# Optimization experiments

Measured on AMD Instinct MI355X. Metric: run time of the kernel, lower is better.

Reference implementation:

```python
import jax, jax.numpy as jnp
import numpy as np

N_NODES = 50000
N_EDGES = 500000
IN_DIM = 64
OUT_DIM = 64
NUM_RELS = 16


def setup_inputs() -> dict:
    key = jax.random.key(0)
    ks = jax.random.split(key, 8)
    h = jax.random.normal(ks[0], (N_NODES, IN_DIM), dtype=jnp.float32)
    he = jax.random.normal(ks[1], (N_EDGES, IN_DIM), dtype=jnp.float32)
    src = jax.random.randint(ks[2], (N_EDGES,), 0, N_NODES)
    dst = jax.random.randint(ks[3], (N_EDGES,), 0, N_NODES)
    rel = jax.random.randint(ks[4], (N_EDGES,), 0, NUM_RELS)
    # xavier-ish scales
    W_shared = jax.random.normal(ks[5], (OUT_DIM, IN_DIM), dtype=jnp.float32) * (2.0 / (IN_DIM + OUT_DIM)) ** 0.5
    W_attn = jax.random.normal(ks[6], (1, 3 * OUT_DIM), dtype=jnp.float32) * (2.0 / (3 * OUT_DIM + 1)) ** 0.5
    W_rel = jax.random.normal(ks[7], (NUM_RELS, IN_DIM, OUT_DIM), dtype=jnp.float32) * (2.0 / (IN_DIM + OUT_DIM)) ** 0.5
    return {"h": h, "he": he, "src": src, "dst": dst, "rel": rel,
            "W_shared": W_shared, "W_attn": W_attn, "W_rel": W_rel}


def reference(h, he, src, dst, rel, W_shared, W_attn, W_rel):
    # --- edge attention: a = attn_fc([z_src, z_edge, z_dst]) (raw linear score, no softmax in original) ---
    Z = h @ W_shared.T                      # [N, out] project all nodes once
    ze = he @ W_shared.T                    # [E, out]
    # split attn weight to avoid materializing [E, 3*out] concat
    Wa_s, Wa_e, Wa_d = jnp.split(W_attn, 3, axis=1)   # each [1, out]
    a = Z[src] @ Wa_s.T + ze @ Wa_e.T + Z[dst] @ Wa_d.T   # [E, 1]
    # --- message: msg = (h_src @ W_rel[rel]) * a ---
    # compute per-(node, relation) transform once [N, R, out], then gather per edge
    H_all = jnp.einsum('ni,rio->nro', h, W_rel)          # [N, R, out]
    msg = H_all[src, rel] * a                             # [E, out]
    # --- scatter-sum aggregation into destination nodes ---
    out = jax.ops.segment_sum(msg, dst, num_segments=N_NODES)  # [N, out]
    # apply_func: activation (relu), no bias
    return jax.nn.relu(out)
```

## Files before the change

kernel.cpp:

```cpp
#include <hip/hip_runtime.h>
#include <math.h>

#define N_NODES 50000
#define N_EDGES 500000
#define NUM_RELS 16
#define GH 64
#define SCAN_BLKS 196
#define AE_BLKS 1954

typedef _Float16 f16x8 __attribute__((ext_vector_type(8)));
typedef _Float16 f16x4 __attribute__((ext_vector_type(4)));
typedef float    f32x4 __attribute__((ext_vector_type(4)));


__global__ void kz(int* __restrict__ c1, int* __restrict__ cu1,
                   int* __restrict__ c2, int* __restrict__ cu2) {
    int i = blockIdx.x * 256 + threadIdx.x;
    if (i < NUM_RELS) { c1[i] = 0; cu1[i] = 0; }
    if (i < N_NODES)  { c2[i] = 0; cu2[i] = 0; }
}

__global__ __launch_bounds__(256) void k_node(
    const float* __restrict__ h, const float4* __restrict__ he4,
    const float* __restrict__ W_shared, const float* __restrict__ W_attn,
    const int* __restrict__ dst, const int* __restrict__ rel,
    float* __restrict__ sn, float* __restrict__ dn,
    int* __restrict__ c1, int* __restrict__ c2,
    _Float16* __restrict__ h_hi, _Float16* __restrict__ h_lo,
    float* __restrict__ edot) {
    __shared__ float sus[64], sud[64], sve[64];
    __shared__ float sdot[256];
    __shared__ int hist[NUM_RELS];
    const int t = threadIdx.x, bid = blockIdx.x;
    const int lane = t & 63;
    const int w = t >> 6;

    const size_t fb = ((size_t)bid * 256 + (size_t)w * 64) * 16;
    const size_t fmax = (size_t)N_EDGES * 16 - 1;
    float4 v[16];
#pragma unroll
    for (int k = 0; k < 16; ++k) {
        size_t fi = fb + (size_t)k * 64 + lane;
        if (fi > fmax) fi = fmax;
        v[k] = he4[fi];
    }

    if (t < 64) {
        float us = 0.f, ud = 0.f, ve = 0.f;
        for (int o = 0; o < 64; ++o) {
            float ww = W_shared[o * 64 + t];
            us = fmaf(ww, W_attn[o],       us);
            ve = fmaf(ww, W_attn[64 + o],  ve);
            ud = fmaf(ww, W_attn[128 + o], ud);
        }
        sus[t] = us; sud[t] = ud; sve[t] = ve;
    }
    if (t < NUM_RELS) hist[t] = 0;
    __syncthreads();

    int n = bid * 256 + t;
    if (bid < SCAN_BLKS && n < N_NODES) {
        const float* hp = h + (size_t)n * 64;
        float s = 0.f, d = 0.f;
#pragma unroll
        for (int i = 0; i < 64; i += 4) {
            float4 hv = *(const float4*)(hp + i);
            s = fmaf(hv.x, sus[i], s);     s = fmaf(hv.y, sus[i + 1], s);
            s = fmaf(hv.z, sus[i + 2], s); s = fmaf(hv.w, sus[i + 3], s);
            d = fmaf(hv.x, sud[i], d);     d = fmaf(hv.y, sud[i + 1], d);
            d = fmaf(hv.z, sud[i + 2], d); d = fmaf(hv.w, sud[i + 3], d);
            f16x4 hi, lo;
            hi[0] = (_Float16)hv.x; lo[0] = (_Float16)(hv.x - (float)hi[0]);
            hi[1] = (_Float16)hv.y; lo[1] = (_Float16)(hv.y - (float)hi[1]);
            hi[2] = (_Float16)hv.z; lo[2] = (_Float16)(hv.z - (float)hi[2]);
            hi[3] = (_Float16)hv.w; lo[3] = (_Float16)(hv.w - (float)hi[3]);
            *(f16x4*)(h_hi + (size_t)n * 64 + i) = hi;
            *(f16x4*)(h_lo + (size_t)n * 64 + i) = lo;
        }
        sn[n] = s; dn[n] = d;
    }

    {
        float4 u = *(const float4*)(sve + 4 * (lane & 15));
#pragma unroll
        for (int k = 0; k < 16; ++k) {
            float p = v[k].x * u.x + v[k].y * u.y + v[k].z * u.z + v[k].w * u.w;
            p += __shfl_xor(p, 1, 64);
            p += __shfl_xor(p, 2, 64);
            p += __shfl_xor(p, 4, 64);
            p += __shfl_xor(p, 8, 64);
            if ((lane & 15) == 0) sdot[w * 64 + k * 4 + (lane >> 4)] = p;
        }
    }
    int e = bid * 256 + t;
    if (e < N_EDGES) edot[e] = sdot[t];

    if (bid < SCAN_BLKS) {
        for (int ee = bid * 256 + t; ee < N_EDGES; ee += SCAN_BLKS * 256) {
            atomicAdd(&hist[rel[ee]], 1);
            atomicAdd(&c2[dst[ee]], 1);
        }
    }
    __syncthreads();
    if (bid < SCAN_BLKS && t < NUM_RELS && hist[t]) atomicAdd(&c1[t], hist[t]);
}

__global__ __launch_bounds__(256) void k_scan1(const int* __restrict__ c2,
                                               int* __restrict__ partial) {
    const int t = threadIdx.x, bid = blockIdx.x;
    const int lane = t & 63, wv = t >> 6;
    __shared__ int ws[4];
    int idx = bid * 256 + t;
    int s = (idx < N_NODES) ? c2[idx] : 0;
#pragma unroll
    for (int off = 32; off > 0; off >>= 1) s += __shfl_xor(s, off, 64);
    if (lane == 0) ws[wv] = s;
    __syncthreads();
    if (t == 0) partial[bid] = ws[0] + ws[1] + ws[2] + ws[3];
}

__global__ __launch_bounds__(256) void k_scan2(const int* __restrict__ partial,
                                               int* __restrict__ pbase,
                                               int* __restrict__ offs2,
                                               const int* __restrict__ c1,
                                               int* __restrict__ offs1) {
    const int t = threadIdx.x;
    const int lane = t & 63, wv = t >> 6;
    __shared__ int wsum[4];
    int v = (t < SCAN_BLKS) ? partial[t] : 0;
    int x = v;
#pragma unroll
    for (int off = 1; off < 64; off <<= 1) {
        int y = __shfl_up(x, off, 64);
        if (lane >= off) x += y;
    }
    if (lane == 63) wsum[wv] = x;
    __syncthreads();
    int wbase = 0;
#pragma unroll
    for (int j = 0; j < 4; ++j) if (j < wv) wbase += wsum[j];
    int excl = wbase + x - v;
    pbase[t] = excl;
    if (t == 255) offs2[N_NODES] = excl;
    if (t == 0) {
        int b = 0;
        for (int r = 0; r < NUM_RELS; ++r) { offs1[r] = b; b += c1[r]; }
        offs1[NUM_RELS] = b;
    }
}

__global__ __launch_bounds__(256) void k_scan3(int* __restrict__ c2,
                                               const int* __restrict__ pbase,
                                               int* __restrict__ offs2) {
    const int t = threadIdx.x, bid = blockIdx.x;
    const int lane = t & 63, wv = t >> 6;
    __shared__ int wsum[4];
    int idx = bid * 256 + t;
    int v = (idx < N_NODES) ? c2[idx] : 0;
    int x = v;
#pragma unroll
    for (int off = 1; off < 64; off <<= 1) {
        int y = __shfl_up(x, off, 64);
        if (lane >= off) x += y;
    }
    if (lane == 63) wsum[wv] = x;
    __syncthreads();
    int wbase = 0;
#pragma unroll
    for (int j = 0; j < 4; ++j) if (j < wv) wbase += wsum[j];
    if (idx < N_NODES) offs2[idx] = pbase[bid] + wbase + x - v;
    if (idx < 4096) c2[idx] = 0;
}

__global__ __launch_bounds__(256) void k_ae(
    const int* __restrict__ src, const int* __restrict__ dst,
    const int* __restrict__ rel, const float* __restrict__ edot,
    const float* __restrict__ sn, const float* __restrict__ dn,
    const int* __restrict__ offs1, int* __restrict__ cur1p,
    const int* __restrict__ offs2, int* __restrict__ cursor2,
    int* __restrict__ srcs, float* __restrict__ aes, int* __restrict__ iperm) {
    __shared__ int hist[NUM_RELS], bbase[NUM_RELS], soffs[NUM_RELS];
    const int t = threadIdx.x;
    const int e = blockIdx.x * 256 + t;
    if (t < NUM_RELS) { hist[t] = 0; soffs[t] = offs1[t]; }
    const bool valid = (e < N_EDGES);
    int r = 0, s_ = 0, d_ = 0;
    float aev = 0.f;
    if (valid) {
        s_ = src[e]; d_ = dst[e]; r = rel[e];
        aev = edot[e] + sn[s_] + dn[d_];
    }
    __syncthreads();
    int lpos = 0;
    if (valid) lpos = atomicAdd(&hist[r], 1);
    __syncthreads();
    if (t < NUM_RELS) bbase[t] = hist[t] ? atomicAdd(&cur1p[t << 8], hist[t]) : 0;
    __syncthreads();
    if (valid) {
        int p1 = soffs[r] + bbase[r] + lpos;
        srcs[p1] = s_; aes[p1] = aev;
        int p2 = offs2[d_] + atomicAdd(&cursor2[d_], 1);
        iperm[p2] = p1;
    }
}

__global__ __launch_bounds__(256, 4) void k_msg(
    const _Float16* __restrict__ h_hi, const _Float16* __restrict__ h_lo,
    const float* __restrict__ W_rel, const int* __restrict__ offs1,
    const int* __restrict__ srcs, const float* __restrict__ aes,
    float* __restrict__ msg)
{
    const int t = threadIdx.x;
    const int lane = t & 63;
    const int quad = lane >> 4;
    const int col  = lane & 15;
    const int wib  = t >> 6;
    const int rh   = blockIdx.x & 31;
    const int r    = rh & 15;
    const int half = rh >> 4;
    const int g    = blockIdx.x >> 5;
    const int wr   = g * 4 + wib;

    const int begin = __builtin_amdgcn_readfirstlane(offs1[r]);
    const int end   = __builtin_amdgcn_readfirstlane(offs1[r + 1]);

    const float* Wb = W_rel + (size_t)r * 4096;
    f16x8 bh[2][2], bl[2][2];
#pragma unroll
    for (int kb = 0; kb < 2; ++kb)
#pragma unroll
        for (int n2 = 0; n2 < 2; ++n2)
#pragma unroll
            for (int j = 0; j < 8; ++j) {
                float w = Wb[(kb * 32 + quad * 8 + j) * 64 + (half * 2 + n2) * 16 + col];
                _Float16 hi = (_Float16)w;
                bh[kb][n2][j] = hi;
                bl[kb][n2][j] = (_Float16)(w - (float)hi);
            }

    for (int base = begin + wr * 16; base < end; base += 256 * 16) {
        int m16 = end - base; if (m16 > 16) m16 = 16;
        const int ridx = base + (col < m16 ? col : m16 - 1);
        const int   sv = srcs[ridx];
        const float av = (col < m16) ? aes[ridx] : 0.f;

        const _Float16* ph = h_hi + (size_t)sv * 64 + quad * 8;
        const _Float16* pl = h_lo + (size_t)sv * 64 + quad * 8;
        f16x8 ah0 = *(const f16x8*)ph, ah1 = *(const f16x8*)(ph + 32);
        f16x8 al0 = *(const f16x8*)pl, al1 = *(const f16x8*)(pl + 32);

        f32x4 acc0 = {0.f, 0.f, 0.f, 0.f};
        f32x4 acc1 = {0.f, 0.f, 0.f, 0.f};
        acc0 = __builtin_amdgcn_mfma_f32_16x16x32_f16(ah0, bh[0][0], acc0, 0, 0, 0);
        acc1 = __builtin_amdgcn_mfma_f32_16x16x32_f16(ah0, bh[0][1], acc1, 0, 0, 0);
        acc0 = __builtin_amdgcn_mfma_f32_16x16x32_f16(ah0, bl[0][0], acc0, 0, 0, 0);
        acc1 = __builtin_amdgcn_mfma_f32_16x16x32_f16(ah0, bl[0][1], acc1, 0, 0, 0);
        acc0 = __builtin_amdgcn_mfma_f32_16x16x32_f16(al0, bh[0][0], acc0, 0, 0, 0);
        acc1 = __builtin_amdgcn_mfma_f32_16x16x32_f16(al0, bh[0][1], acc1, 0, 0, 0);
        acc0 = __builtin_amdgcn_mfma_f32_16x16x32_f16(ah1, bh[1][0], acc0, 0, 0, 0);
        acc1 = __builtin_amdgcn_mfma_f32_16x16x32_f16(ah1, bh[1][1], acc1, 0, 0, 0);
        acc0 = __builtin_amdgcn_mfma_f32_16x16x32_f16(ah1, bl[1][0], acc0, 0, 0, 0);
        acc1 = __builtin_amdgcn_mfma_f32_16x16x32_f16(ah1, bl[1][1], acc1, 0, 0, 0);
        acc0 = __builtin_amdgcn_mfma_f32_16x16x32_f16(al1, bh[1][0], acc0, 0, 0, 0);
        acc1 = __builtin_amdgcn_mfma_f32_16x16x32_f16(al1, bh[1][1], acc1, 0, 0, 0);

#pragma unroll
        for (int reg = 0; reg < 4; ++reg) {
            const int m = quad * 4 + reg;
            const float am = __shfl(av, m, 64);
            if (m < m16) {
                float* op = msg + (size_t)(base + m) * 64 + half * 32 + col;
                op[0]  = am * acc0[reg];
                op[16] = am * acc1[reg];
            }
        }
    }
}

__global__ __launch_bounds__(256) void k_out(
    const float* __restrict__ msg, const int* __restrict__ iperm,
    const int* __restrict__ offs2, float* __restrict__ out)
{
    const int lane = threadIdx.x & 63;
    const int gw   = blockIdx.x * 4 + (threadIdx.x >> 6);
    const int nw   = gridDim.x * 4;
    for (int n = gw; n < N_NODES; n += nw) {
        const int qb = offs2[n], qe = offs2[n + 1];
        float s0 = 0.f, s1 = 0.f, s2 = 0.f, s3 = 0.f;
        int q = qb;
        for (; q + 4 <= qe; q += 4) {
            int p0 = iperm[q], p1 = iperm[q + 1], p2 = iperm[q + 2], p3 = iperm[q + 3];
            s0 += msg[(size_t)p0 * 64 + lane];
            s1 += msg[(size_t)p1 * 64 + lane];
            s2 += msg[(size_t)p2 * 64 + lane];
            s3 += msg[(size_t)p3 * 64 + lane];
        }
        for (; q < qe; ++q)
            s0 += msg[(size_t)iperm[q] * 64 + lane];
        float s = (s0 + s1) + (s2 + s3);
        out[(size_t)n * 64 + lane] = fmaxf(s, 0.f);
    }
}

extern "C" void kernel_launch(void* const* d_in, const int* in_sizes, int n_in,
                              void* d_out, int out_size, void* d_ws, size_t ws_size,
                              hipStream_t stream) {
    const float*  h        = (const float*)d_in[0];
    const float4* he4      = (const float4*)d_in[1];
    const int*    src      = (const int*)d_in[2];
    const int*    dst      = (const int*)d_in[3];
    const int*    rel      = (const int*)d_in[4];
    const float*  W_shared = (const float*)d_in[5];
    const float*  W_attn   = (const float*)d_in[6];
    const float*  W_rel    = (const float*)d_in[7];
    float*        out      = (float*)d_out;

    int*      counts1 = (int*)d_ws + 0;
    int*      cursor1 = (int*)d_ws + 16;
    int*      offs1   = (int*)d_ws + 32;
    int*      counts2 = (int*)d_ws + 64;
    int*      cursor2 = (int*)d_ws + 50064;
    int*      offs2   = (int*)d_ws + 100064;
    float*    sn      = (float*)d_ws + 150080;
    float*    dn      = (float*)d_ws + 200080;
    int*      srcs    = (int*)d_ws + 250080;
    float*    aes     = (float*)d_ws + 750080;
    int*      iperm   = (int*)d_ws + 1250080;
    _Float16* h_hi    = (_Float16*)((int*)d_ws + 1750080);
    _Float16* h_lo    = (_Float16*)((int*)d_ws + 3350080);
    float*    edot    = (float*)d_ws + 4950080;
    int*      partial = srcs;
    int*      pbase   = srcs + 256;
    float*    msg     = (float*)d_in[1];

    kz<<<(N_NODES + 255) / 256, 256, 0, stream>>>(counts1, cursor1, counts2, cursor2);
    k_node<<<AE_BLKS, 256, 0, stream>>>(h, he4, W_shared, W_attn, dst, rel,
                                        sn, dn, counts1, counts2, h_hi, h_lo, edot);
    k_scan1<<<SCAN_BLKS, 256, 0, stream>>>(counts2, partial);
    k_scan2<<<1, 256, 0, stream>>>(partial, pbase, offs2, counts1, offs1);
    k_scan3<<<SCAN_BLKS, 256, 0, stream>>>(counts2, pbase, offs2);
    k_ae<<<AE_BLKS, 256, 0, stream>>>(src, dst, rel, edot, sn, dn,
                                      offs1, counts2, offs2, cursor2, srcs, aes, iperm);
    k_msg<<<32 * GH, 256, 0, stream>>>(h_hi, h_lo, W_rel, offs1, srcs, aes, msg);
    k_out<<<2048, 256, 0, stream>>>(msg, iperm, offs2, out);
}
```

Baseline: 356.3 us.

## Replace global dst atomics with LDS-packed byte histograms per edge slice

The destination counting sort no longer uses global atomics on per-node counters. Each of 128 blocks builds an LDS histogram of its edge slice, packing four byte counters into each int. A column pass then builds per-slice base offsets, and a second slice pass scatters iperm using LDS atomics. The goal is to remove contended global atomics, at the cost of extra kernels and byte-sized scratch written into the he input buffer. Byte counters overflow if one slice sends more than 255 edges to the same node.

```diff
diff --git a/kernel.cpp b/kernel.cpp
--- a/kernel.cpp
+++ b/kernel.cpp
@@ -7,30 +7,26 @@
 #define GH 64
 #define SCAN_BLKS 196
 #define AE_BLKS 1954
+#define HG 128
+#define HSLICE 3907
 
 typedef _Float16 f16x8 __attribute__((ext_vector_type(8)));
 typedef _Float16 f16x4 __attribute__((ext_vector_type(4)));
 typedef float    f32x4 __attribute__((ext_vector_type(4)));
 
 
-__global__ void kz(int* __restrict__ c1, int* __restrict__ cu1,
-                   int* __restrict__ c2, int* __restrict__ cu2) {
-    int i = blockIdx.x * 256 + threadIdx.x;
-    if (i < NUM_RELS) { c1[i] = 0; cu1[i] = 0; }
-    if (i < N_NODES)  { c2[i] = 0; cu2[i] = 0; }
-}
-
-__global__ __launch_bounds__(256) void k_node(
+__global__ void kz(int* __restrict__ w0) {
+    w0[blockIdx.x * 256 + threadIdx.x] = 0;
+}
+
+__global__ __launch_bounds__(256, 2) void k_node(
     const float* __restrict__ h, const float4* __restrict__ he4,
     const float* __restrict__ W_shared, const float* __restrict__ W_attn,
-    const int* __restrict__ dst, const int* __restrict__ rel,
     float* __restrict__ sn, float* __restrict__ dn,
-    int* __restrict__ c1, int* __restrict__ c2,
     _Float16* __restrict__ h_hi, _Float16* __restrict__ h_lo,
     float* __restrict__ edot) {
     __shared__ float sus[64], sud[64], sve[64];
     __shared__ float sdot[256];
-    __shared__ int hist[NUM_RELS];
     const int t = threadIdx.x, bid = blockIdx.x;
     const int lane = t & 63;
     const int w = t >> 6;
@@ -47,6 +43,7 @@
 
     if (t < 64) {
         float us = 0.f, ud = 0.f, ve = 0.f;
+#pragma unroll 8
         for (int o = 0; o < 64; ++o) {
             float ww = W_shared[o * 64 + t];
             us = fmaf(ww, W_attn[o],       us);
@@ -55,7 +52,6 @@
         }
         sus[t] = us; sud[t] = ud; sve[t] = ve;
     }
-    if (t < NUM_RELS) hist[t] = 0;
     __syncthreads();
 
     int n = bid * 256 + t;
@@ -94,15 +90,49 @@
     }
     int e = bid * 256 + t;
     if (e < N_EDGES) edot[e] = sdot[t];
-
-    if (bid < SCAN_BLKS) {
-        for (int ee = bid * 256 + t; ee < N_EDGES; ee += SCAN_BLKS * 256) {
-            atomicAdd(&hist[rel[ee]], 1);
-            atomicAdd(&c2[dst[ee]], 1);
-        }
-    }
-    __syncthreads();
-    if (bid < SCAN_BLKS && t < NUM_RELS && hist[t]) atomicAdd(&c1[t], hist[t]);
+}
+
+__global__ __launch_bounds__(256) void k_histA(
+    const int* __restrict__ dst, const int* __restrict__ rel,
+    unsigned char* __restrict__ h_b, int* __restrict__ c1p) {
+    __shared__ int cnt[12500];
+    __shared__ int relh[NUM_RELS];
+    const int t = threadIdx.x, blk = blockIdx.x;
+    for (int w = t; w < 12500; w += 256) cnt[w] = 0;
+    if (t < NUM_RELS) relh[t] = 0;
+    __syncthreads();
+    const int s0 = blk * HSLICE;
+    const int s1 = (s0 + HSLICE < N_EDGES) ? s0 + HSLICE : N_EDGES;
+    for (int e = s0 + t; e < s1; e += 256) {
+        int d = dst[e];
+        atomicAdd(&cnt[d >> 2], 1 << ((d & 3) * 8));
+        atomicAdd(&relh[rel[e]], 1);
+    }
+    __syncthreads();
+    uchar4* hb4 = (uchar4*)(h_b + (size_t)blk * 50000);
+    for (int w = t; w < 12500; w += 256) {
+        int v = cnt[w];
+        hb4[w] = make_uchar4((unsigned char)(v & 255),
+                             (unsigned char)((v >> 8) & 255),
+                             (unsigned char)((v >> 16) & 255),
+                             (unsigned char)((v >> 24) & 255));
+    }
+    if (t < NUM_RELS && relh[t]) atomicAdd(&c1p[t << 10], relh[t]);
+}
+
+__global__ __launch_bounds__(256) void k_sumB(
+    const unsigned char* __restrict__ h_b, unsigned char* __restrict__ base8,
+    int* __restrict__ c2) {
+    int b = blockIdx.x * 256 + threadIdx.x;
+    if (b >= N_NODES) return;
+    int run = 0;
+#pragma unroll 8
+    for (int k = 0; k < HG; ++k) {
+        int v = h_b[(size_t)k * 50000 + b];
+        base8[(size_t)k * 50000 + b] = (unsigned char)run;
+        run += v;
+    }
+    c2[b] = run;
 }
 
 __global__ __launch_bounds__(256) void k_scan1(const int* __restrict__ c2,
@@ -122,7 +152,7 @@
 __global__ __launch_bounds__(256) void k_scan2(const int* __restrict__ partial,
                                                int* __restrict__ pbase,
                                                int* __restrict__ offs2,
-                                               const int* __restrict__ c1,
+                                               const int* __restrict__ c1p,
                                                int* __restrict__ offs1) {
     const int t = threadIdx.x;
     const int lane = t & 63, wv = t >> 6;
@@ -144,12 +174,12 @@
     if (t == 255) offs2[N_NODES] = excl;
     if (t == 0) {
         int b = 0;
-        for (int r = 0; r < NUM_RELS; ++r) { offs1[r] = b; b += c1[r]; }
+        for (int r = 0; r < NUM_RELS; ++r) { offs1[r] = b; b += c1p[r << 10]; }
         offs1[NUM_RELS] = b;
     }
 }
 
-__global__ __launch_bounds__(256) void k_scan3(int* __restrict__ c2,
+__global__ __launch_bounds__(256) void k_scan3(const int* __restrict__ c2,
                                                const int* __restrict__ pbase,
                                                int* __restrict__ offs2) {
     const int t = threadIdx.x, bid = blockIdx.x;
@@ -169,7 +199,6 @@
 #pragma unroll
     for (int j = 0; j < 4; ++j) if (j < wv) wbase += wsum[j];
     if (idx < N_NODES) offs2[idx] = pbase[bid] + wbase + x - v;
-    if (idx < 4096) c2[idx] = 0;
 }
 
 __global__ __launch_bounds__(256) void k_ae(
@@ -177,30 +206,48 @@
     const int* __restrict__ rel, const float* __restrict__ edot,
     const float* __restrict__ sn, const float* __restrict__ dn,
     const int* __restrict__ offs1, int* __restrict__ cur1p,
-    const int* __restrict__ offs2, int* __restrict__ cursor2,
-    int* __restrict__ srcs, float* __restrict__ aes, int* __restrict__ iperm) {
+    int* __restrict__ srcs, float* __restrict__ aes, int* __restrict__ pos1) {
     __shared__ int hist[NUM_RELS], bbase[NUM_RELS], soffs[NUM_RELS];
     const int t = threadIdx.x;
     const int e = blockIdx.x * 256 + t;
     if (t < NUM_RELS) { hist[t] = 0; soffs[t] = offs1[t]; }
     const bool valid = (e < N_EDGES);
-    int r = 0, s_ = 0, d_ = 0;
+    int r = 0, s_ = 0;
     float aev = 0.f;
     if (valid) {
-        s_ = src[e]; d_ = dst[e]; r = rel[e];
+        s_ = src[e]; int d_ = dst[e]; r = rel[e];
         aev = edot[e] + sn[s_] + dn[d_];
     }
     __syncthreads();
     int lpos = 0;
     if (valid) lpos = atomicAdd(&hist[r], 1);
     __syncthreads();
-    if (t < NUM_RELS) bbase[t] = hist[t] ? atomicAdd(&cur1p[t << 8], hist[t]) : 0;
+    if (t < NUM_RELS) bbase[t] = hist[t] ? atomicAdd(&cur1p[t << 10], hist[t]) : 0;
     __syncthreads();
     if (valid) {
         int p1 = soffs[r] + bbase[r] + lpos;
         srcs[p1] = s_; aes[p1] = aev;
-        int p2 = offs2[d_] + atomicAdd(&cursor2[d_], 1);
-        iperm[p2] = p1;
+        pos1[e] = p1;
+    }
+}
+
+__global__ __launch_bounds__(256) void k_scatC(
+    const int* __restrict__ dst, const int* __restrict__ pos1,
+    const int* __restrict__ offs2, const unsigned char* __restrict__ base8,
+    int* __restrict__ iperm) {
+    __shared__ int cnt[12500];
+    const int t = threadIdx.x, blk = blockIdx.x;
+    for (int w = t; w < 12500; w += 256) cnt[w] = 0;
+    __syncthreads();
+    const int s0 = blk * HSLICE;
+    const int s1 = (s0 + HSLICE < N_EDGES) ? s0 + HSLICE : N_EDGES;
+    const unsigned char* bb = base8 + (size_t)blk * 50000;
+    for (int e = s0 + t; e < s1; e += 256) {
+        int d = dst[e];
+        int old = atomicAdd(&cnt[d >> 2], 1 << ((d & 3) * 8));
+        int lr = (old >> ((d & 3) * 8)) & 255;
+        int p2 = offs2[d] + (int)bb[d] + lr;
+        iperm[p2] = pos1[e];
     }
 }
 
@@ -315,32 +362,37 @@
     const float*  W_rel    = (const float*)d_in[7];
     float*        out      = (float*)d_out;
 
-    int*      counts1 = (int*)d_ws + 0;
-    int*      cursor1 = (int*)d_ws + 16;
-    int*      offs1   = (int*)d_ws + 32;
-    int*      counts2 = (int*)d_ws + 64;
-    int*      cursor2 = (int*)d_ws + 50064;
-    int*      offs2   = (int*)d_ws + 100064;
-    float*    sn      = (float*)d_ws + 150080;
-    float*    dn      = (float*)d_ws + 200080;
-    int*      srcs    = (int*)d_ws + 250080;
-    float*    aes     = (float*)d_ws + 750080;
-    int*      iperm   = (int*)d_ws + 1250080;
-    _Float16* h_hi    = (_Float16*)((int*)d_ws + 1750080);
-    _Float16* h_lo    = (_Float16*)((int*)d_ws + 3350080);
-    float*    edot    = (float*)d_ws + 4950080;
+    int*      c1p     = (int*)d_ws + 0;
+    int*      cur1p   = (int*)d_ws + 16384;
+    int*      offs1   = (int*)d_ws + 32768;
+    int*      c2      = (int*)d_ws + 32800;
+    int*      offs2   = (int*)d_ws + 82800;
+    float*    sn      = (float*)d_ws + 132864;
+    float*    dn      = (float*)d_ws + 182864;
+    int*      srcs    = (int*)d_ws + 232864;
+    float*    aes     = (float*)d_ws + 732864;
+    int*      iperm   = (int*)d_ws + 1232864;
+    int*      pos1    = (int*)d_ws + 1732864;
+    float*    edot    = (float*)d_ws + 2232864;
+    _Float16* h_hi    = (_Float16*)((int*)d_ws + 2732864);
+    _Float16* h_lo    = (_Float16*)((int*)d_ws + 4332864);
     int*      partial = srcs;
     int*      pbase   = srcs + 256;
+    unsigned char* h_b   = (unsigned char*)d_in[1];
+    unsigned char* base8 = (unsigned char*)d_in[1] + 6400000;
     float*    msg     = (float*)d_in[1];
 
-    kz<<<(N_NODES + 255) / 256, 256, 0, stream>>>(counts1, cursor1, counts2, cursor2);
-    k_node<<<AE_BLKS, 256, 0, stream>>>(h, he4, W_shared, W_attn, dst, rel,
-                                        sn, dn, counts1, counts2, h_hi, h_lo, edot);
-    k_scan1<<<SCAN_BLKS, 256, 0, stream>>>(counts2, partial);
-    k_scan2<<<1, 256, 0, stream>>>(partial, pbase, offs2, counts1, offs1);
-    k_scan3<<<SCAN_BLKS, 256, 0, stream>>>(counts2, pbase, offs2);
+    kz<<<128, 256, 0, stream>>>((int*)d_ws);
+    k_node<<<AE_BLKS, 256, 0, stream>>>(h, he4, W_shared, W_attn,
+                                        sn, dn, h_hi, h_lo, edot);
+    k_histA<<<HG, 256, 0, stream>>>(dst, rel, h_b, c1p);
+    k_sumB<<<SCAN_BLKS, 256, 0, stream>>>(h_b, base8, c2);
+    k_scan1<<<SCAN_BLKS, 256, 0, stream>>>(c2, partial);
+    k_scan2<<<1, 256, 0, stream>>>(partial, pbase, offs2, c1p, offs1);
+    k_scan3<<<SCAN_BLKS, 256, 0, stream>>>(c2, pbase, offs2);
     k_ae<<<AE_BLKS, 256, 0, stream>>>(src, dst, rel, edot, sn, dn,
-                                      offs1, counts2, offs2, cursor2, srcs, aes, iperm);
+                                      offs1, cur1p, srcs, aes, pos1);
+    k_scatC<<<HG, 256, 0, stream>>>(dst, pos1, offs2, base8, iperm);
     k_msg<<<32 * GH, 256, 0, stream>>>(h_hi, h_lo, W_rel, offs1, srcs, aes, msg);
     k_out<<<2048, 256, 0, stream>>>(msg, iperm, offs2, out);
 }
```

Result: slower. 366.4 us (+2.9%).
